# Kernel tuning notes

Measured on AMD Instinct MI355X. Metric: run time of the kernel, lower is better.

The kernel has to match this reference:

```python
import jax, jax.numpy as jnp
import numpy as np

N_NODES = 50000
N_EDGES = 800000
F_IN = 11
HID = 128
HEADS = 4
N_ACT = 6
NEG_SLOPE = 0.2


def _gat_layer(x, W, a_src, a_dst, b, src, dst, heads, out_dim):
    # x: [N, Fin]; W: [Fin, heads*out]; a_src/a_dst: [heads, out]; b: [heads*out]
    N = x.shape[0]
    h = (x @ W).reshape(N, heads, out_dim)                     # [N,H,C]
    alpha_src = jnp.einsum('nhc,hc->nh', h, a_src)             # [N,H]
    alpha_dst = jnp.einsum('nhc,hc->nh', h, a_dst)             # [N,H]
    e = jax.nn.leaky_relu(alpha_src[src] + alpha_dst[dst], NEG_SLOPE)  # [E,H]
    # segment softmax over incoming edges of each dst node
    m = jax.ops.segment_max(e, dst, num_segments=N)            # [N,H]
    ex = jnp.exp(e - m[dst])
    s = jax.ops.segment_sum(ex, dst, num_segments=N)           # [N,H]
    alpha = ex / s[dst]                                        # [E,H]
    msg = h[src] * alpha[..., None]                            # [E,H,C]
    agg = jax.ops.segment_sum(msg, dst, num_segments=N)        # [N,H,C]
    return agg.reshape(N, heads * out_dim) + b


def setup_inputs() -> dict:
    key = jax.random.key(0)
    ks = jax.random.split(key, 24)
    f32 = jnp.float32
    p = {}
    p['x'] = jax.random.normal(ks[0], (N_NODES, F_IN), dtype=f32)
    p['edge_index'] = jax.random.randint(ks[1], (2, N_EDGES), 0, N_NODES, dtype=jnp.int64)
    p['current_node_idx'] = 0
    def w(k, shape):
        return (jax.random.normal(k, shape, dtype=f32) * 0.1)
    p['W1'] = w(ks[2], (F_IN, HEADS * HID)); p['as1'] = w(ks[3], (HEADS, HID))
    p['ad1'] = w(ks[4], (HEADS, HID)); p['b1'] = jnp.zeros((HEADS * HID,), f32)
    p['W2'] = w(ks[5], (HEADS * HID, HEADS * HID)); p['as2'] = w(ks[6], (HEADS, HID))
    p['ad2'] = w(ks[7], (HEADS, HID)); p['b2'] = jnp.zeros((HEADS * HID,), f32)
    # layer 3: 512 -> 128, 1 head
    p['W3'] = w(ks[8], (HEADS * HID, HID)); p['as3'] = w(ks[9], (1, HID))
    p['ad3'] = w(ks[10], (1, HID)); p['b3'] = jnp.zeros((HID,), f32)
    # policy head
    p['pw1'] = w(ks[11], (HID, HID)); p['pb1'] = jnp.zeros((HID,), f32)
    p['pw2'] = w(ks[12], (HID, N_ACT)); p['pb2'] = jnp.zeros((N_ACT,), f32)
    # value head
    p['vw1'] = w(ks[13], (HID, HID)); p['vb1'] = jnp.zeros((HID,), f32)
    p['vw2'] = w(ks[14], (HID, 1)); p['vb2'] = jnp.zeros((1,), f32)
    return p


def reference(x, edge_index, current_node_idx,
              W1, as1, ad1, b1, W2, as2, ad2, b2, W3, as3, ad3, b3,
              pw1, pb1, pw2, pb2, vw1, vb1, vw2, vb2):
    src, dst = edge_index[0], edge_index[1]
    h = _gat_layer(x, W1, as1, ad1, b1, src, dst, HEADS, HID)
    h = jax.nn.elu(h)
    h = _gat_layer(h, W2, as2, ad2, b2, src, dst, HEADS, HID)
    h = jax.nn.elu(h)
    h = _gat_layer(h, W3, as3, ad3, b3, src, dst, 1, HID)      # [N, HID]
    graph_emb = h.mean(axis=0, keepdims=True)                  # [1, HID]
    combined = graph_emb + h[current_node_idx]                 # [1, HID]
    p = jax.nn.relu(combined @ pw1 + pb1) @ pw2 + pb2          # [1, N_ACT]
    v = jax.nn.relu(combined @ vw1 + vb1) @ vw2 + vb2          # [1, 1]
    return p, v
```

## Files before the change

kernel.cpp:

```cpp
#include <hip/hip_runtime.h>
#include <math.h>

#define NN 50000
#define NE 800000
#define F_IN 11
#define HID 128
#define NEG_SLOPE 0.2f

typedef __attribute__((ext_vector_type(8))) short short8;
typedef __attribute__((ext_vector_type(4))) float f32x4;

__device__ __forceinline__ float bf2f(ushort u) {
  return __uint_as_float(((unsigned)u) << 16);
}
__device__ __forceinline__ ushort f2bf(float f) {
  unsigned u = __float_as_uint(f);
  return (ushort)((u + 0x7fff + ((u >> 16) & 1)) >> 16);
}
__device__ __forceinline__ float lrelu(float x) { return x > 0.f ? x : NEG_SLOPE * x; }
__device__ __forceinline__ float elu1(float x) { return x > 0.f ? x : expm1f(x); }

#define MNEG (-1e30f)

__device__ __forceinline__ void wave_fence() {
  asm volatile("s_waitcnt lgkmcnt(0)" ::: "memory");
}

#define AS1 __attribute__((address_space(1)))
#define AS3 __attribute__((address_space(3)))

__global__ void k_deg(const int* __restrict__ ei, int* __restrict__ deg) {
  int e = blockIdx.x * blockDim.x + threadIdx.x;
  if (e < NE) atomicAdd(&deg[ei[NE + e]], 1);
}

__global__ void k_scan(const int* __restrict__ deg, int* __restrict__ row_ptr,
                       int* __restrict__ cursor) {
  const int T = 1024;
  const int CH = (NN + T - 1) / T;
  __shared__ int ssum[T];
  int t = threadIdx.x;
  int base = t * CH;
  int s = 0;
  for (int i = 0; i < CH; i++) {
    int idx = base + i;
    if (idx < NN) s += deg[idx];
  }
  ssum[t] = s;
  __syncthreads();
  for (int off = 1; off < T; off <<= 1) {
    int v = (t >= off) ? ssum[t - off] : 0;
    __syncthreads();
    ssum[t] += v;
    __syncthreads();
  }
  int run = ssum[t] - s;
  for (int i = 0; i < CH; i++) {
    int idx = base + i;
    if (idx < NN) {
      row_ptr[idx] = run;
      cursor[idx] = run;
      run += deg[idx];
    }
  }
  if (t == 0) row_ptr[NN] = ssum[T - 1];
}

__global__ void k_scatter(const int* __restrict__ ei, int* __restrict__ cursor,
                          int* __restrict__ csr_src) {
  int e = blockIdx.x * blockDim.x + threadIdx.x;
  if (e < NE) {
    int d = ei[NE + e];
    int pos = atomicAdd(&cursor[d], 1);
    csr_src[pos] = ei[e];
  }
}

__global__ void k_wt(const float* __restrict__ W, ushort* __restrict__ Wt, int K, int N) {
  __shared__ float tl[32][33];
  int bn = blockIdx.x * 32, bk = blockIdx.y * 32;
  int tx = threadIdx.x & 31, ty = threadIdx.x >> 5;
  for (int i = ty; i < 32; i += 8) tl[i][tx] = W[(size_t)(bk + i) * N + bn + tx];
  __syncthreads();
  for (int i = ty; i < 32; i += 8)
    Wt[(size_t)(bn + i) * K + bk + tx] = f2bf(tl[tx][i]);
}

__global__ void k_vsd(const float* __restrict__ W1, const float* __restrict__ as1,
                      const float* __restrict__ ad1, float* __restrict__ vs,
                      float* __restrict__ vd) {
  int t = threadIdx.x;
  if (t >= 88) return;
  int side = t & 1, kh = t >> 1;
  int k = kh >> 2, h = kh & 3;
  const float* av = side ? ad1 : as1;
  float s = 0.f;
  for (int c = 0; c < HID; c++) s += W1[k * 512 + h * HID + c] * av[h * HID + c];
  (side ? vd : vs)[kh] = s;
}

__global__ void k_ax(const float* __restrict__ x, const float* __restrict__ vs,
                     const float* __restrict__ vd, float* __restrict__ asrc,
                     float* __restrict__ adst) {
  int n = blockIdx.x * blockDim.x + threadIdx.x;
  if (n >= NN) return;
  float xr[F_IN];
#pragma unroll
  for (int k = 0; k < F_IN; k++) xr[k] = x[n * F_IN + k];
  float s[4] = {}, dd[4] = {};
#pragma unroll
  for (int k = 0; k < F_IN; k++)
#pragma unroll
    for (int h = 0; h < 4; h++) {
      s[h] += xr[k] * vs[k * 4 + h];
      dd[h] += xr[k] * vd[k * 4 + h];
    }
  *(f32x4*)(asrc + n * 4) = f32x4{s[0], s[1], s[2], s[3]};
  *(f32x4*)(adst + n * 4) = f32x4{dd[0], dd[1], dd[2], dd[3]};
}

__global__ __launch_bounds__(256) void k_aggpre(
    const float* __restrict__ x, const float* __restrict__ asrc,
    const float* __restrict__ adst, const int* __restrict__ row_ptr,
    const int* __restrict__ csr_src, float* __restrict__ P) {
  const int CAP = 64;
  __shared__ int src_c[4][CAP];
  __shared__ float ea[4][CAP * 4];
  int t = threadIdx.x, lane = t & 63, wv = t >> 6;
  int d = blockIdx.x * 4 + wv;
  int start = row_ptr[d], deg = row_ptr[d + 1] - start;
  int dcap = min(deg, CAP);
  for (int i = lane; i < dcap; i += 64) src_c[wv][i] = csr_src[start + i];
  wave_fence();
  int hh = lane & 3;
  float adh = adst[d * 4 + hh];
  float m = MNEG, s = 0.f;
  int deg4 = deg * 4;
  for (int i = lane; i < deg4; i += 64) {
    int k = i >> 2;
    int sn = (k < CAP) ? src_c[wv][k] : csr_src[start + k];
    float v = lrelu(asrc[sn * 4 + hh] + adh);
    if (k < CAP) ea[wv][i] = v;
    float nm = fmaxf(m, v);
    s = s * __expf(m - nm) + __expf(v - nm);
    m = nm;
  }
#pragma unroll
  for (int off = 4; off < 64; off <<= 1) {
    float m2 = __shfl_xor(m, off);
    float s2 = __shfl_xor(s, off);
    float nm = fmaxf(m, m2);
    s = s * __expf(m - nm) + s2 * __expf(m2 - nm);
    m = nm;
  }
  float sinv = (s > 0.f) ? 1.f / s : 0.f;
  int dc4 = dcap * 4;
  for (int i = lane; i < dc4; i += 64) ea[wv][i] = __expf(ea[wv][i] - m) * sinv;
  wave_fence();
  int hq = lane / F_IN;
  int k = lane - hq * F_IN;
  int h = hq & 3;
  float mh = __shfl(m, h), sih = __shfl(sinv, h);
  float adh2 = adst[d * 4 + h];
  float acc = 0.f;
  for (int e = 0; e < deg; e++) {
    int sn;
    float a;
    if (e < CAP) {
      sn = src_c[wv][e];
      a = ea[wv][e * 4 + h];
    } else {
      sn = csr_src[start + e];
      a = __expf(lrelu(asrc[sn * 4 + h] + adh2) - mh) * sih;
    }
    acc += a * x[sn * F_IN + k];
  }
  if (lane < 44) P[(size_t)d * 44 + lane] = acc;
}

__global__ __launch_bounds__(256) void k_gemm_l1(
    const float* __restrict__ P, const float* __restrict__ W1,
    const float* __restrict__ b1, ushort* __restrict__ out) {
  __shared__ float sW[F_IN * 512];
  __shared__ float sP[16][44];
  int t = threadIdx.x;
  for (int i = t; i < F_IN * 512; i += 256) sW[i] = W1[i];
  int n0 = blockIdx.x * 16;
  for (int i = t; i < 16 * 44; i += 256)
    sP[i / 44][i % 44] = P[(size_t)(n0 + i / 44) * 44 + (i % 44)];
  __syncthreads();
  int j0 = 2 * t;
  int h = j0 >> 7;
  float b0 = b1[j0], bb = b1[j0 + 1];
  float w0[F_IN], w1v[F_IN];
#pragma unroll
  for (int k = 0; k < F_IN; k++) {
    w0[k] = sW[k * 512 + j0];
    w1v[k] = sW[k * 512 + j0 + 1];
  }
  for (int nn = 0; nn < 16; nn++) {
    float a0 = b0, a1 = bb;
#pragma unroll
    for (int k = 0; k < F_IN; k++) {
      float pv = sP[nn][h * F_IN + k];
      a0 += pv * w0[k];
      a1 += pv * w1v[k];
    }
    a0 = elu1(a0);
    a1 = elu1(a1);
    unsigned pk = (unsigned)f2bf(a0) | ((unsigned)f2bf(a1) << 16);
    *(unsigned*)(out + (size_t)(n0 + nn) * 512 + j0) = pk;
  }
}

#define TM 128
#define TN 128
#define TK 64
__global__ __launch_bounds__(256) void k_mfma(const ushort* __restrict__ A,
                                              const ushort* __restrict__ Bt,
                                              ushort* __restrict__ C,
                                              int M, int N, int K) {
  __shared__ ushort lds[TM * TK + TN * TK];
  ushort* As = lds;
  ushort* Bs = lds + TM * TK;
  int tid = threadIdx.x;
  int lane = tid & 63, wv = tid >> 6;
  int wr = wv >> 1, wc = wv & 1;
  int bm0 = blockIdx.x * TM, bn0 = blockIdx.y * TN;
  int l15 = lane & 15, l4 = lane >> 4;
  f32x4 acc[4][4] = {};
  for (int k0 = 0; k0 < K; k0 += TK) {
#pragma unroll
    for (int it = 0; it < 4; ++it) {
      int chunk = it * 4 + wv;
      int pbase = chunk * 1024;
      int p = pbase + lane * 16;
      int prow = p >> 7;
      int lblk = ((p >> 4) & 7) ^ (prow & 7);
      int gr = bm0 + prow;
      gr = gr < M ? gr : M - 1;
      __builtin_amdgcn_global_load_lds(
          (const AS1 void*)(A + (size_t)gr * K + (k0 + lblk * 8)),
          (AS3 void*)((char*)As + pbase), 16, 0, 0);
      int gb = bn0 + prow;
      __builtin_amdgcn_global_load_lds(
          (const AS1 void*)(Bt + (size_t)gb * K + (k0 + lblk * 8)),
          (AS3 void*)((char*)Bs + pbase), 16, 0, 0);
    }
    __syncthreads();
#pragma unroll
    for (int kk = 0; kk < 2; ++kk) {
      int cb = kk * 4 + l4;
      short8 af[4], bfr[4];
#pragma unroll
      for (int m = 0; m < 4; ++m) {
        int row = wr * 64 + m * 16 + l15;
        af[m] = *(const short8*)((const char*)As + row * 128 + ((cb ^ (row & 7)) << 4));
      }
#pragma unroll
      for (int n = 0; n < 4; ++n) {
        int row = wc * 64 + n * 16 + l15;
        bfr[n] = *(const short8*)((const char*)Bs + row * 128 + ((cb ^ (row & 7)) << 4));
      }
#pragma unroll
      for (int m = 0; m < 4; ++m)
#pragma unroll
        for (int n = 0; n < 4; ++n)
          acc[m][n] = __builtin_amdgcn_mfma_f32_16x16x32_bf16(af[m], bfr[n], acc[m][n], 0, 0, 0);
    }
    __syncthreads();
  }
#pragma unroll
  for (int m = 0; m < 4; ++m) {
#pragma unroll
    for (int r = 0; r < 4; ++r) {
      int row = bm0 + wr * 64 + m * 16 + l4 * 4 + r;
      if (row < M) {
#pragma unroll
        for (int n = 0; n < 4; ++n) {
          int col = bn0 + wc * 64 + n * 16 + l15;
          C[(size_t)row * N + col] = f2bf(acc[m][n][r]);
        }
      }
    }
  }
}

template <int H>
__global__ void k_alpha(const ushort* __restrict__ h, const float* __restrict__ a_src,
                        const float* __restrict__ a_dst, float* __restrict__ asrc,
                        float* __restrict__ adst) {
  int t = threadIdx.x;
  int lane = t & 63;
  int n_g, h_g;
  if (H == 4) {
    n_g = blockIdx.x * 4 + (t >> 6);
    h_g = lane >> 4;
  } else {
    n_g = blockIdx.x * 16 + (t >> 4);
    h_g = 0;
  }
  if (n_g >= NN) return;
  int cl = lane & 15;
  short8 hv = *(const short8*)(h + (size_t)n_g * (H * 128) + h_g * 128 + cl * 8);
  const float* as = a_src + h_g * 128 + cl * 8;
  const float* ad = a_dst + h_g * 128 + cl * 8;
  float s1 = 0.f, s2 = 0.f;
#pragma unroll
  for (int j = 0; j < 8; j++) {
    float v = bf2f((ushort)hv[j]);
    s1 += v * as[j];
    s2 += v * ad[j];
  }
#pragma unroll
  for (int off = 1; off < 16; off <<= 1) {
    s1 += __shfl_xor(s1, off);
    s2 += __shfl_xor(s2, off);
  }
  if (cl == 0) {
    asrc[n_g * H + h_g] = s1;
    adst[n_g * H + h_g] = s2;
  }
}

__global__ __launch_bounds__(256) void k_agg4w(
    const ushort* __restrict__ h, const float* __restrict__ asrc,
    const float* __restrict__ adst, const int* __restrict__ row_ptr,
    const int* __restrict__ csr_src, const float* __restrict__ bias,
    ushort* __restrict__ out) {
  const int CAP = 64;
  __shared__ int src_c[4][CAP];
  __shared__ float ea[4][CAP * 4];
  int t = threadIdx.x, lane = t & 63, wv = t >> 6;
  int d = blockIdx.x * 4 + wv;
  int start = row_ptr[d], deg = row_ptr[d + 1] - start;
  int dcap = min(deg, CAP);
  for (int i = lane; i < dcap; i += 64) src_c[wv][i] = csr_src[start + i];
  wave_fence();
  int hh = lane & 3;
  float adh = adst[d * 4 + hh];
  float m = MNEG, s = 0.f;
  int deg4 = deg * 4;
  for (int i = lane; i < deg4; i += 64) {
    int k = i >> 2;
    int sn = (k < CAP) ? src_c[wv][k] : csr_src[start + k];
    float v = lrelu(asrc[sn * 4 + hh] + adh);
    if (k < CAP) ea[wv][i] = v;
    float nm = fmaxf(m, v);
    s = s * __expf(m - nm) + __expf(v - nm);
    m = nm;
  }
#pragma unroll
  for (int off = 4; off < 64; off <<= 1) {
    float m2 = __shfl_xor(m, off);
    float s2 = __shfl_xor(s, off);
    float nm = fmaxf(m, m2);
    s = s * __expf(m - nm) + s2 * __expf(m2 - nm);
    m = nm;
  }
  float sinv = (s > 0.f) ? 1.f / s : 0.f;
  int dc4 = dcap * 4;
  for (int i = lane; i < dc4; i += 64) ea[wv][i] = __expf(ea[wv][i] - m) * sinv;
  wave_fence();
  int hl = lane >> 4;
  float mh = __shfl(m, hl), sih = __shfl(sinv, hl);
  float adh2 = adst[d * 4 + hl];
  float acc[8] = {};
  for (int k = 0; k < deg; k++) {
    int sn;
    float a;
    if (k < CAP) {
      sn = src_c[wv][k];
      a = ea[wv][k * 4 + hl];
    } else {
      sn = csr_src[start + k];
      a = __expf(lrelu(asrc[sn * 4 + hl] + adh2) - mh) * sih;
    }
    short8 hv = *(const short8*)(h + (size_t)sn * 512 + lane * 8);
#pragma unroll
    for (int j = 0; j < 8; j++) acc[j] += a * bf2f((ushort)hv[j]);
  }
  const float* bp = bias + lane * 8;
  unsigned pk[4];
#pragma unroll
  for (int j = 0; j < 4; j++) {
    float o0 = elu1(acc[2 * j] + bp[2 * j]);
    float o1 = elu1(acc[2 * j + 1] + bp[2 * j + 1]);
    pk[j] = (unsigned)f2bf(o0) | ((unsigned)f2bf(o1) << 16);
  }
  *(uint4*)(out + (size_t)d * 512 + lane * 8) = make_uint4(pk[0], pk[1], pk[2], pk[3]);
}

__global__ __launch_bounds__(256) void k_agg1w(
    const ushort* __restrict__ h, const float* __restrict__ asrc,
    const float* __restrict__ adst, const int* __restrict__ row_ptr,
    const int* __restrict__ csr_src, const float* __restrict__ bias,
    ushort* __restrict__ out) {
  const int CAP = 64;
  __shared__ int src_c[4][CAP];
  __shared__ float ea[4][CAP];
  int t = threadIdx.x, lane = t & 63, wv = t >> 6;
  int d = blockIdx.x * 4 + wv;
  int start = row_ptr[d], deg = row_ptr[d + 1] - start;
  int dcap = min(deg, CAP);
  for (int i = lane; i < dcap; i += 64) src_c[wv][i] = csr_src[start + i];
  wave_fence();
  float adh = adst[d];
  float m = MNEG, s = 0.f;
  for (int i = lane; i < deg; i += 64) {
    int sn = (i < CAP) ? src_c[wv][i] : csr_src[start + i];
    float v = lrelu(asrc[sn] + adh);
    if (i < CAP) ea[wv][i] = v;
    float nm = fmaxf(m, v);
    s = s * __expf(m - nm) + __expf(v - nm);
    m = nm;
  }
#pragma unroll
  for (int off = 1; off < 64; off <<= 1) {
    float m2 = __shfl_xor(m, off);
    float s2 = __shfl_xor(s, off);
    float nm = fmaxf(m, m2);
    s = s * __expf(m - nm) + s2 * __expf(m2 - nm);
    m = nm;
  }
  float sinv = (s > 0.f) ? 1.f / s : 0.f;
  for (int i = lane; i < dcap; i += 64) ea[wv][i] = __expf(ea[wv][i] - m) * sinv;
  wave_fence();
  float acc0 = 0.f, acc1 = 0.f;
  for (int k = 0; k < deg; k++) {
    int sn;
    float a;
    if (k < CAP) {
      sn = src_c[wv][k];
      a = ea[wv][k];
    } else {
      sn = csr_src[start + k];
      a = __expf(lrelu(asrc[sn] + adh) - m) * sinv;
    }
    unsigned hv = *(const unsigned*)(h + (size_t)sn * 128 + lane * 2);
    acc0 += a * bf2f((ushort)(hv & 0xffff));
    acc1 += a * bf2f((ushort)(hv >> 16));
  }
  float o0 = acc0 + bias[lane * 2];
  float o1 = acc1 + bias[lane * 2 + 1];
  unsigned pk = (unsigned)f2bf(o0) | ((unsigned)f2bf(o1) << 16);
  *(unsigned*)(out + (size_t)d * 128 + lane * 2) = pk;
}

__global__ __launch_bounds__(256) void k_colsum(const ushort* __restrict__ h3,
                                                float* __restrict__ gsum) {
  __shared__ float partial[16 * 128];
  int t = threadIdx.x;
  int rg = t >> 4, cl = t & 15;
  int nb = gridDim.x;
  int per = (NN + nb - 1) / nb;
  int r0 = blockIdx.x * per, r1 = min(NN, r0 + per);
  float acc[8] = {};
  for (int r = r0 + rg; r < r1; r += 16) {
    short8 hv = *(const short8*)(h3 + (size_t)r * 128 + cl * 8);
#pragma unroll
    for (int j = 0; j < 8; j++) acc[j] += bf2f((ushort)hv[j]);
  }
#pragma unroll
  for (int j = 0; j < 8; j++) partial[rg * 128 + cl * 8 + j] = acc[j];
  __syncthreads();
  if (t < 128) {
    float s = 0.f;
    for (int q = 0; q < 16; q++) s += partial[q * 128 + t];
    atomicAdd(&gsum[t], s);
  }
}

__global__ void k_head(const float* __restrict__ gsum, const ushort* __restrict__ h3,
                       const int* __restrict__ curp, const float* __restrict__ pw1,
                       const float* __restrict__ pb1, const float* __restrict__ pw2,
                       const float* __restrict__ pb2, const float* __restrict__ vw1,
                       const float* __restrict__ vb1, const float* __restrict__ vw2,
                       const float* __restrict__ vb2, float* __restrict__ outp) {
  __shared__ float comb[HID], ph[HID], vh[HID];
  int t = threadIdx.x;
  int cur = curp[0];
  comb[t] = gsum[t] * (1.f / NN) + bf2f(h3[(size_t)cur * HID + t]);
  __syncthreads();
  float accp = pb1[t], accv = vb1[t];
  for (int k = 0; k < HID; k++) {
    float cv = comb[k];
    accp += cv * pw1[k * HID + t];
    accv += cv * vw1[k * HID + t];
  }
  ph[t] = fmaxf(accp, 0.f);
  vh[t] = fmaxf(accv, 0.f);
  __syncthreads();
  if (t < 6) {
    float a = pb2[t];
    for (int k = 0; k < HID; k++) a += ph[k] * pw2[k * 6 + t];
    outp[t] = a;
  }
  if (t == 6) {
    float a = vb2[0];
    for (int k = 0; k < HID; k++) a += vh[k] * vw2[k];
    outp[6] = a;
  }
}

extern "C" void kernel_launch(void* const* d_in, const int* in_sizes, int n_in,
                              void* d_out, int out_size, void* d_ws, size_t ws_size,
                              hipStream_t stream) {
  const float* x = (const float*)d_in[0];
  const int* ei = (const int*)d_in[1];
  const int* cur = (const int*)d_in[2];
  const float* W1 = (const float*)d_in[3];
  const float* as1 = (const float*)d_in[4];
  const float* ad1 = (const float*)d_in[5];
  const float* b1 = (const float*)d_in[6];
  const float* W2 = (const float*)d_in[7];
  const float* as2 = (const float*)d_in[8];
  const float* ad2 = (const float*)d_in[9];
  const float* b2 = (const float*)d_in[10];
  const float* W3 = (const float*)d_in[11];
  const float* as3 = (const float*)d_in[12];
  const float* ad3 = (const float*)d_in[13];
  const float* b3 = (const float*)d_in[14];
  const float* pw1 = (const float*)d_in[15];
  const float* pb1 = (const float*)d_in[16];
  const float* pw2 = (const float*)d_in[17];
  const float* pb2 = (const float*)d_in[18];
  const float* vw1 = (const float*)d_in[19];
  const float* vb1 = (const float*)d_in[20];
  const float* vw2 = (const float*)d_in[21];
  const float* vb2 = (const float*)d_in[22];
  float* out = (float*)d_out;

  char* w = (char*)d_ws;
  ushort* G = (ushort*)w;    w += (size_t)NN * 512 * 2;
  ushort* Abuf = (ushort*)w; w += (size_t)NN * 512 * 2;
  ushort* Wt2 = (ushort*)w;  w += (size_t)512 * 512 * 2;
  ushort* Wt3 = (ushort*)w;  w += (size_t)128 * 512 * 2;
  float* P = (float*)w;      w += (size_t)NN * 44 * 4;
  float* asrc = (float*)w;   w += (size_t)NN * 4 * 4;
  float* adst = (float*)w;   w += (size_t)NN * 4 * 4;
  int* deg = (int*)w;        w += (size_t)NN * 4;
  int* cursor = (int*)w;     w += (size_t)NN * 4;
  int* row_ptr = (int*)w;    w += (size_t)(NN + 1) * 4;
  int* csr_src = (int*)w;    w += (size_t)NE * 4;
  float* gsum = (float*)w;   w += (size_t)HID * 4;
  float* vs = (float*)w;     w += 44 * 4;
  float* vd = (float*)w;     w += 44 * 4;

  hipMemsetAsync(deg, 0, NN * 4, stream);
  hipMemsetAsync(gsum, 0, HID * 4, stream);

  k_deg<<<(NE + 255) / 256, 256, 0, stream>>>(ei, deg);
  k_scan<<<1, 1024, 0, stream>>>(deg, row_ptr, cursor);
  k_scatter<<<(NE + 255) / 256, 256, 0, stream>>>(ei, cursor, csr_src);

  k_wt<<<dim3(512 / 32, 512 / 32), 256, 0, stream>>>(W2, Wt2, 512, 512);
  k_wt<<<dim3(128 / 32, 512 / 32), 256, 0, stream>>>(W3, Wt3, 512, 128);

  const int GB = (NN + TM - 1) / TM;

  k_vsd<<<1, 128, 0, stream>>>(W1, as1, ad1, vs, vd);
  k_ax<<<(NN + 255) / 256, 256, 0, stream>>>(x, vs, vd, asrc, adst);
  k_aggpre<<<NN / 4, 256, 0, stream>>>(x, asrc, adst, row_ptr, csr_src, P);
  k_gemm_l1<<<NN / 16, 256, 0, stream>>>(P, W1, b1, Abuf);

  k_mfma<<<dim3(GB, 4), 256, 0, stream>>>(Abuf, Wt2, G, NN, 512, 512);
  k_alpha<4><<<(NN + 3) / 4, 256, 0, stream>>>(G, as2, ad2, asrc, adst);
  k_agg4w<<<NN / 4, 256, 0, stream>>>(G, asrc, adst, row_ptr, csr_src, b2, Abuf);

  k_mfma<<<dim3(GB, 1), 256, 0, stream>>>(Abuf, Wt3, G, NN, 128, 512);
  k_alpha<1><<<(NN + 15) / 16, 256, 0, stream>>>(G, as3, ad3, asrc, adst);
  k_agg1w<<<NN / 4, 256, 0, stream>>>(G, asrc, adst, row_ptr, csr_src, b3, Abuf);

  k_colsum<<<256, 256, 0, stream>>>(Abuf, gsum);
  k_head<<<1, 128, 0, stream>>>(gsum, Abuf, cur, pw1, pb1, pw2, pb2, vw1, vb1, vw2, vb2, out);
}
```

Before: 668.5 us.

## Fuse attention-logit computation into MFMA GEMM epilogue, remap blocks per XCD, unroll aggregation

The separate k_alpha kernels are removed. The attention source/destination dot products are now computed in the MFMA GEMM epilogue from the fp32 accumulators, reduced across lanes and waves through shared memory, and written directly. The GEMM grid becomes 1D with an XCD-aware block remap so that neighbouring tiles land on the same XCD for L2 reuse. The aggregation loops in k_agg4w and k_agg1w are unrolled by two with dual accumulators so more gathers are in flight. This saves a kernel launch and a full re-read of G per layer. In exchange it adds epilogue shuffles and extra registers, and the logits are now computed from unrounded fp32 values rather than from the bf16 output.

After: 680.0 us. Within noise of the previous version (+1.7%).

```diff
diff --git a/kernel.cpp b/kernel.cpp
--- a/kernel.cpp
+++ b/kernel.cpp
@@ -216,17 +216,25 @@
 #define TM 128
 #define TN 128
 #define TK 64
-__global__ __launch_bounds__(256) void k_mfma(const ushort* __restrict__ A,
-                                              const ushort* __restrict__ Bt,
-                                              ushort* __restrict__ C,
-                                              int M, int N, int K) {
+template <int H>
+__global__ __launch_bounds__(256) void k_mfma(
+    const ushort* __restrict__ A, const ushort* __restrict__ Bt,
+    ushort* __restrict__ C, const float* __restrict__ a_srcv,
+    const float* __restrict__ a_dstv, float* __restrict__ asrc,
+    float* __restrict__ adst, int M, int N, int K) {
   __shared__ ushort lds[TM * TK + TN * TK];
+  __shared__ float sal[128][2], sad[128][2];
   ushort* As = lds;
   ushort* Bs = lds + TM * TK;
   int tid = threadIdx.x;
   int lane = tid & 63, wv = tid >> 6;
   int wr = wv >> 1, wc = wv & 1;
-  int bm0 = blockIdx.x * TM, bn0 = blockIdx.y * TN;
+  int nwg = gridDim.x;
+  int q = nwg >> 3, rr = nwg & 7;
+  int xcd = blockIdx.x & 7, off8 = blockIdx.x >> 3;
+  int lid = (xcd < rr ? xcd * (q + 1) : rr * (q + 1) + (xcd - rr) * q) + off8;
+  int bm = lid / H, hy = lid - bm * H;
+  int bm0 = bm * TM, bn0 = hy * TN;
   int l15 = lane & 15, l4 = lane >> 4;
   f32x4 acc[4][4] = {};
   for (int k0 = 0; k0 < K; k0 += TK) {
@@ -284,42 +292,43 @@
       }
     }
   }
-}
-
-template <int H>
-__global__ void k_alpha(const ushort* __restrict__ h, const float* __restrict__ a_src,
-                        const float* __restrict__ a_dst, float* __restrict__ asrc,
-                        float* __restrict__ adst) {
-  int t = threadIdx.x;
-  int lane = t & 63;
-  int n_g, h_g;
-  if (H == 4) {
-    n_g = blockIdx.x * 4 + (t >> 6);
-    h_g = lane >> 4;
-  } else {
-    n_g = blockIdx.x * 16 + (t >> 4);
-    h_g = 0;
-  }
-  if (n_g >= NN) return;
-  int cl = lane & 15;
-  short8 hv = *(const short8*)(h + (size_t)n_g * (H * 128) + h_g * 128 + cl * 8);
-  const float* as = a_src + h_g * 128 + cl * 8;
-  const float* ad = a_dst + h_g * 128 + cl * 8;
-  float s1 = 0.f, s2 = 0.f;
-#pragma unroll
-  for (int j = 0; j < 8; j++) {
-    float v = bf2f((ushort)hv[j]);
-    s1 += v * as[j];
-    s2 += v * ad[j];
-  }
-#pragma unroll
-  for (int off = 1; off < 16; off <<= 1) {
-    s1 += __shfl_xor(s1, off);
-    s2 += __shfl_xor(s2, off);
-  }
-  if (cl == 0) {
-    asrc[n_g * H + h_g] = s1;
-    adst[n_g * H + h_g] = s2;
+  float asv[4], adv[4];
+#pragma unroll
+  for (int n = 0; n < 4; ++n) {
+    int c = hy * 128 + wc * 64 + n * 16 + l15;
+    asv[n] = a_srcv[c];
+    adv[n] = a_dstv[c];
+  }
+#pragma unroll
+  for (int m = 0; m < 4; ++m) {
+#pragma unroll
+    for (int r = 0; r < 4; ++r) {
+      float s1 = 0.f, s2 = 0.f;
+#pragma unroll
+      for (int n = 0; n < 4; ++n) {
+        float cv = acc[m][n][r];
+        s1 += cv * asv[n];
+        s2 += cv * adv[n];
+      }
+#pragma unroll
+      for (int off = 1; off < 16; off <<= 1) {
+        s1 += __shfl_xor(s1, off);
+        s2 += __shfl_xor(s2, off);
+      }
+      if (l15 == 0) {
+        int rb = wr * 64 + m * 16 + l4 * 4 + r;
+        sal[rb][wc] = s1;
+        sad[rb][wc] = s2;
+      }
+    }
+  }
+  __syncthreads();
+  if (tid < 128) {
+    int gr = bm0 + tid;
+    if (gr < M) {
+      asrc[gr * H + hy] = sal[tid][0] + sal[tid][1];
+      adst[gr * H + hy] = sad[tid][0] + sad[tid][1];
+    }
   }
 }
 
@@ -365,8 +374,33 @@
   int hl = lane >> 4;
   float mh = __shfl(m, hl), sih = __shfl(sinv, hl);
   float adh2 = adst[d * 4 + hl];
-  float acc[8] = {};
-  for (int k = 0; k < deg; k++) {
+  float acc0[8] = {}, acc1[8] = {};
+  int k = 0;
+  for (; k + 2 <= deg; k += 2) {
+    int sn0, sn1;
+    float a0, a1;
+    if (k < CAP) {
+      sn0 = src_c[wv][k];
+      a0 = ea[wv][k * 4 + hl];
+    } else {
+      sn0 = csr_src[start + k];
+      a0 = __expf(lrelu(asrc[sn0 * 4 + hl] + adh2) - mh) * sih;
+    }
+    if (k + 1 < CAP) {
+      sn1 = src_c[wv][k + 1];
+      a1 = ea[wv][(k + 1) * 4 + hl];
+    } else {
+      sn1 = csr_src[start + k + 1];
+      a1 = __expf(lrelu(asrc[sn1 * 4 + hl] + adh2) - mh) * sih;
+    }
+    short8 v0 = *(const short8*)(h + (size_t)sn0 * 512 + lane * 8);
+    short8 v1 = *(const short8*)(h + (size_t)sn1 * 512 + lane * 8);
+#pragma unroll
+    for (int j = 0; j < 8; j++) acc0[j] += a0 * bf2f((ushort)v0[j]);
+#pragma unroll
+    for (int j = 0; j < 8; j++) acc1[j] += a1 * bf2f((ushort)v1[j]);
+  }
+  if (k < deg) {
     int sn;
     float a;
     if (k < CAP) {
@@ -376,16 +410,16 @@
       sn = csr_src[start + k];
       a = __expf(lrelu(asrc[sn * 4 + hl] + adh2) - mh) * sih;
     }
-    short8 hv = *(const short8*)(h + (size_t)sn * 512 + lane * 8);
-#pragma unroll
-    for (int j = 0; j < 8; j++) acc[j] += a * bf2f((ushort)hv[j]);
+    short8 v0 = *(const short8*)(h + (size_t)sn * 512 + lane * 8);
+#pragma unroll
+    for (int j = 0; j < 8; j++) acc0[j] += a * bf2f((ushort)v0[j]);
   }
   const float* bp = bias + lane * 8;
   unsigned pk[4];
 #pragma unroll
   for (int j = 0; j < 4; j++) {
-    float o0 = elu1(acc[2 * j] + bp[2 * j]);
-    float o1 = elu1(acc[2 * j + 1] + bp[2 * j + 1]);
+    float o0 = elu1(acc0[2 * j] + acc1[2 * j] + bp[2 * j]);
+    float o1 = elu1(acc0[2 * j + 1] + acc1[2 * j + 1] + bp[2 * j + 1]);
     pk[j] = (unsigned)f2bf(o0) | ((unsigned)f2bf(o1) << 16);
   }
   *(uint4*)(out + (size_t)d * 512 + lane * 8) = make_uint4(pk[0], pk[1], pk[2], pk[3]);
@@ -426,23 +460,48 @@
   float sinv = (s > 0.f) ? 1.f / s : 0.f;
   for (int i = lane; i < dcap; i += 64) ea[wv][i] = __expf(ea[wv][i] - m) * sinv;
   wave_fence();
-  float acc0 = 0.f, acc1 = 0.f;
-  for (int k = 0; k < deg; k++) {
+  float a00 = 0.f, a01 = 0.f, a10 = 0.f, a11 = 0.f;
+  int k = 0;
+  for (; k + 2 <= deg; k += 2) {
+    int sn0, sn1;
+    float w0, w1;
+    if (k < CAP) {
+      sn0 = src_c[wv][k];
+      w0 = ea[wv][k];
+    } else {
+      sn0 = csr_src[start + k];
+      w0 = __expf(lrelu(asrc[sn0] + adh) - m) * sinv;
+    }
+    if (k + 1 < CAP) {
+      sn1 = src_c[wv][k + 1];
+      w1 = ea[wv][k + 1];
+    } else {
+      sn1 = csr_src[start + k + 1];
+      w1 = __expf(lrelu(asrc[sn1] + adh) - m) * sinv;
+    }
+    unsigned h0 = *(const unsigned*)(h + (size_t)sn0 * 128 + lane * 2);
+    unsigned h1 = *(const unsigned*)(h + (size_t)sn1 * 128 + lane * 2);
+    a00 += w0 * bf2f((ushort)(h0 & 0xffff));
+    a01 += w0 * bf2f((ushort)(h0 >> 16));
+    a10 += w1 * bf2f((ushort)(h1 & 0xffff));
+    a11 += w1 * bf2f((ushort)(h1 >> 16));
+  }
+  if (k < deg) {
     int sn;
-    float a;
+    float w0;
     if (k < CAP) {
       sn = src_c[wv][k];
-      a = ea[wv][k];
+      w0 = ea[wv][k];
     } else {
       sn = csr_src[start + k];
-      a = __expf(lrelu(asrc[sn] + adh) - m) * sinv;
-    }
-    unsigned hv = *(const unsigned*)(h + (size_t)sn * 128 + lane * 2);
-    acc0 += a * bf2f((ushort)(hv & 0xffff));
-    acc1 += a * bf2f((ushort)(hv >> 16));
-  }
-  float o0 = acc0 + bias[lane * 2];
-  float o1 = acc1 + bias[lane * 2 + 1];
+      w0 = __expf(lrelu(asrc[sn] + adh) - m) * sinv;
+    }
+    unsigned h0 = *(const unsigned*)(h + (size_t)sn * 128 + lane * 2);
+    a00 += w0 * bf2f((ushort)(h0 & 0xffff));
+    a01 += w0 * bf2f((ushort)(h0 >> 16));
+  }
+  float o0 = a00 + a10 + bias[lane * 2];
+  float o1 = a01 + a11 + bias[lane * 2 + 1];
   unsigned pk = (unsigned)f2bf(o0) | ((unsigned)f2bf(o1) << 16);
   *(unsigned*)(out + (size_t)d * 128 + lane * 2) = pk;
 }
@@ -564,12 +623,10 @@
   k_aggpre<<<NN / 4, 256, 0, stream>>>(x, asrc, adst, row_ptr, csr_src, P);
   k_gemm_l1<<<NN / 16, 256, 0, stream>>>(P, W1, b1, Abuf);
 
-  k_mfma<<<dim3(GB, 4), 256, 0, stream>>>(Abuf, Wt2, G, NN, 512, 512);
-  k_alpha<4><<<(NN + 3) / 4, 256, 0, stream>>>(G, as2, ad2, asrc, adst);
+  k_mfma<4><<<GB * 4, 256, 0, stream>>>(Abuf, Wt2, G, as2, ad2, asrc, adst, NN, 512, 512);
   k_agg4w<<<NN / 4, 256, 0, stream>>>(G, asrc, adst, row_ptr, csr_src, b2, Abuf);
 
-  k_mfma<<<dim3(GB, 1), 256, 0, stream>>>(Abuf, Wt3, G, NN, 128, 512);
-  k_alpha<1><<<(NN + 15) / 16, 256, 0, stream>>>(G, as3, ad3, asrc, adst);
+  k_mfma<1><<<GB, 256, 0, stream>>>(Abuf, Wt3, G, as3, ad3, asrc, adst, NN, 128, 512);
   k_agg1w<<<NN / 4, 256, 0, stream>>>(G, asrc, adst, row_ptr, csr_src, b3, Abuf);
 
   k_colsum<<<256, 256, 0, stream>>>(Abuf, gsum);
```

## Unroll edge gathers for memory-level parallelism and split layer-3 edges across lane groups

Applied to the files above, without the earlier changes.

The per-destination aggregation loops in the layer-1 pre-aggregation and the 4-head aggregation are unrolled by four, so four independent gathers are in flight per iteration, with separate accumulators in the 4-head kernel. The single-head aggregation is reorganised so each wave handles four edges at once: 16 lanes each read 16 bytes per edge, and the partial sums are combined with cross-lane shuffles. The layer-1 GEMM now processes 64 nodes per block instead of 16, spreading the shared-memory weight load over more rows. In exchange the kernels use more registers, which may lower occupancy, and the single-head kernel adds a shuffle reduction.

After: 671.6 us. No clear change (+0.5%).

```diff
diff --git a/kernel.cpp b/kernel.cpp
--- a/kernel.cpp
+++ b/kernel.cpp
@@ -163,18 +163,38 @@
   float mh = __shfl(m, h), sih = __shfl(sinv, h);
   float adh2 = adst[d * 4 + h];
   float acc = 0.f;
-  for (int e = 0; e < deg; e++) {
+#define GETP(i, SN, A)                                                \
+  do {                                                                \
+    int kk_ = e + (i);                                                \
+    if (kk_ < CAP) {                                                  \
+      SN = src_c[wv][kk_];                                            \
+      A = ea[wv][kk_ * 4 + h];                                        \
+    } else {                                                          \
+      SN = csr_src[start + kk_];                                      \
+      A = __expf(lrelu(asrc[SN * 4 + h] + adh2) - mh) * sih;          \
+    }                                                                 \
+  } while (0)
+  int e = 0;
+  for (; e + 4 <= deg; e += 4) {
+    int sn0, sn1, sn2, sn3;
+    float a0, a1, a2, a3;
+    GETP(0, sn0, a0);
+    GETP(1, sn1, a1);
+    GETP(2, sn2, a2);
+    GETP(3, sn3, a3);
+    float x0 = x[sn0 * F_IN + k];
+    float x1 = x[sn1 * F_IN + k];
+    float x2 = x[sn2 * F_IN + k];
+    float x3 = x[sn3 * F_IN + k];
+    acc += a0 * x0 + a1 * x1 + a2 * x2 + a3 * x3;
+  }
+  for (; e < deg; e++) {
     int sn;
     float a;
-    if (e < CAP) {
-      sn = src_c[wv][e];
-      a = ea[wv][e * 4 + h];
-    } else {
-      sn = csr_src[start + e];
-      a = __expf(lrelu(asrc[sn * 4 + h] + adh2) - mh) * sih;
-    }
+    GETP(0, sn, a);
     acc += a * x[sn * F_IN + k];
   }
+#undef GETP
   if (lane < 44) P[(size_t)d * 44 + lane] = acc;
 }
 
@@ -182,12 +202,14 @@
     const float* __restrict__ P, const float* __restrict__ W1,
     const float* __restrict__ b1, ushort* __restrict__ out) {
   __shared__ float sW[F_IN * 512];
-  __shared__ float sP[16][44];
+  __shared__ float sP[64][44];
   int t = threadIdx.x;
   for (int i = t; i < F_IN * 512; i += 256) sW[i] = W1[i];
-  int n0 = blockIdx.x * 16;
-  for (int i = t; i < 16 * 44; i += 256)
-    sP[i / 44][i % 44] = P[(size_t)(n0 + i / 44) * 44 + (i % 44)];
+  int n0 = blockIdx.x * 64;
+  for (int i = t; i < 64 * 44; i += 256) {
+    int nn = i / 44, kk = i % 44;
+    sP[nn][kk] = (n0 + nn < NN) ? P[(size_t)(n0 + nn) * 44 + kk] : 0.f;
+  }
   __syncthreads();
   int j0 = 2 * t;
   int h = j0 >> 7;
@@ -198,7 +220,8 @@
     w0[k] = sW[k * 512 + j0];
     w1v[k] = sW[k * 512 + j0 + 1];
   }
-  for (int nn = 0; nn < 16; nn++) {
+  for (int nn = 0; nn < 64; nn++) {
+    if (n0 + nn >= NN) break;
     float a0 = b0, a1 = bb;
 #pragma unroll
     for (int k = 0; k < F_IN; k++) {
@@ -365,27 +388,55 @@
   int hl = lane >> 4;
   float mh = __shfl(m, hl), sih = __shfl(sinv, hl);
   float adh2 = adst[d * 4 + hl];
-  float acc[8] = {};
-  for (int k = 0; k < deg; k++) {
+#define GET4(i, SN, A)                                                \
+  do {                                                                \
+    int kk_ = k + (i);                                                \
+    if (kk_ < CAP) {                                                  \
+      SN = src_c[wv][kk_];                                            \
+      A = ea[wv][kk_ * 4 + hl];                                       \
+    } else {                                                          \
+      SN = csr_src[start + kk_];                                      \
+      A = __expf(lrelu(asrc[SN * 4 + hl] + adh2) - mh) * sih;         \
+    }                                                                 \
+  } while (0)
+  float acc0[8] = {}, acc1[8] = {}, acc2[8] = {}, acc3[8] = {};
+  int k = 0;
+  for (; k + 4 <= deg; k += 4) {
+    int sn0, sn1, sn2, sn3;
+    float a0, a1, a2, a3;
+    GET4(0, sn0, a0);
+    GET4(1, sn1, a1);
+    GET4(2, sn2, a2);
+    GET4(3, sn3, a3);
+    short8 v0 = *(const short8*)(h + (size_t)sn0 * 512 + lane * 8);
+    short8 v1 = *(const short8*)(h + (size_t)sn1 * 512 + lane * 8);
+    short8 v2 = *(const short8*)(h + (size_t)sn2 * 512 + lane * 8);
+    short8 v3 = *(const short8*)(h + (size_t)sn3 * 512 + lane * 8);
+#pragma unroll
+    for (int j = 0; j < 8; j++) acc0[j] += a0 * bf2f((ushort)v0[j]);
+#pragma unroll
+    for (int j = 0; j < 8; j++) acc1[j] += a1 * bf2f((ushort)v1[j]);
+#pragma unroll
+    for (int j = 0; j < 8; j++) acc2[j] += a2 * bf2f((ushort)v2[j]);
+#pragma unroll
+    for (int j = 0; j < 8; j++) acc3[j] += a3 * bf2f((ushort)v3[j]);
+  }
+  for (; k < deg; k++) {
     int sn;
     float a;
-    if (k < CAP) {
-      sn = src_c[wv][k];
-      a = ea[wv][k * 4 + hl];
-    } else {
-      sn = csr_src[start + k];
-      a = __expf(lrelu(asrc[sn * 4 + hl] + adh2) - mh) * sih;
-    }
-    short8 hv = *(const short8*)(h + (size_t)sn * 512 + lane * 8);
-#pragma unroll
-    for (int j = 0; j < 8; j++) acc[j] += a * bf2f((ushort)hv[j]);
-  }
+    GET4(0, sn, a);
+    short8 v0 = *(const short8*)(h + (size_t)sn * 512 + lane * 8);
+#pragma unroll
+    for (int j = 0; j < 8; j++) acc0[j] += a * bf2f((ushort)v0[j]);
+  }
+#undef GET4
   const float* bp = bias + lane * 8;
   unsigned pk[4];
 #pragma unroll
   for (int j = 0; j < 4; j++) {
-    float o0 = elu1(acc[2 * j] + bp[2 * j]);
-    float o1 = elu1(acc[2 * j + 1] + bp[2 * j + 1]);
+    float o0 = elu1(acc0[2 * j] + acc1[2 * j] + acc2[2 * j] + acc3[2 * j] + bp[2 * j]);
+    float o1 = elu1(acc0[2 * j + 1] + acc1[2 * j + 1] + acc2[2 * j + 1] + acc3[2 * j + 1] +
+                    bp[2 * j + 1]);
     pk[j] = (unsigned)f2bf(o0) | ((unsigned)f2bf(o1) << 16);
   }
   *(uint4*)(out + (size_t)d * 512 + lane * 8) = make_uint4(pk[0], pk[1], pk[2], pk[3]);
@@ -400,6 +451,7 @@
   __shared__ int src_c[4][CAP];
   __shared__ float ea[4][CAP];
   int t = threadIdx.x, lane = t & 63, wv = t >> 6;
+  int slot = lane >> 4, cl = lane & 15;
   int d = blockIdx.x * 4 + wv;
   int start = row_ptr[d], deg = row_ptr[d + 1] - start;
   int dcap = min(deg, CAP);
@@ -426,25 +478,57 @@
   float sinv = (s > 0.f) ? 1.f / s : 0.f;
   for (int i = lane; i < dcap; i += 64) ea[wv][i] = __expf(ea[wv][i] - m) * sinv;
   wave_fence();
-  float acc0 = 0.f, acc1 = 0.f;
-  for (int k = 0; k < deg; k++) {
+#define GET1(KK, SN, A)                                               \
+  do {                                                                \
+    if ((KK) < CAP) {                                                 \
+      SN = src_c[wv][KK];                                             \
+      A = ea[wv][KK];                                                 \
+    } else {                                                          \
+      SN = csr_src[start + (KK)];                                     \
+      A = __expf(lrelu(asrc[SN] + adh) - m) * sinv;                   \
+    }                                                                 \
+  } while (0)
+  float acc0[8] = {}, acc1[8] = {};
+  int k = slot;
+  for (; k + 4 < deg; k += 8) {
+    int sn0, sn1;
+    float a0, a1;
+    GET1(k, sn0, a0);
+    GET1(k + 4, sn1, a1);
+    short8 v0 = *(const short8*)(h + (size_t)sn0 * 128 + cl * 8);
+    short8 v1 = *(const short8*)(h + (size_t)sn1 * 128 + cl * 8);
+#pragma unroll
+    for (int j = 0; j < 8; j++) acc0[j] += a0 * bf2f((ushort)v0[j]);
+#pragma unroll
+    for (int j = 0; j < 8; j++) acc1[j] += a1 * bf2f((ushort)v1[j]);
+  }
+  for (; k < deg; k += 4) {
     int sn;
     float a;
-    if (k < CAP) {
-      sn = src_c[wv][k];
-      a = ea[wv][k];
-    } else {
-      sn = csr_src[start + k];
-      a = __expf(lrelu(asrc[sn] + adh) - m) * sinv;
+    GET1(k, sn, a);
+    short8 v0 = *(const short8*)(h + (size_t)sn * 128 + cl * 8);
+#pragma unroll
+    for (int j = 0; j < 8; j++) acc0[j] += a * bf2f((ushort)v0[j]);
+  }
+#undef GET1
+#pragma unroll
+  for (int j = 0; j < 8; j++) {
+    float v = acc0[j] + acc1[j];
+    v += __shfl_xor(v, 16);
+    v += __shfl_xor(v, 32);
+    acc0[j] = v;
+  }
+  if (slot == 0) {
+    const float* bp = bias + cl * 8;
+    unsigned pk[4];
+#pragma unroll
+    for (int j = 0; j < 4; j++) {
+      float o0 = acc0[2 * j] + bp[2 * j];
+      float o1 = acc0[2 * j + 1] + bp[2 * j + 1];
+      pk[j] = (unsigned)f2bf(o0) | ((unsigned)f2bf(o1) << 16);
     }
-    unsigned hv = *(const unsigned*)(h + (size_t)sn * 128 + lane * 2);
-    acc0 += a * bf2f((ushort)(hv & 0xffff));
-    acc1 += a * bf2f((ushort)(hv >> 16));
-  }
-  float o0 = acc0 + bias[lane * 2];
-  float o1 = acc1 + bias[lane * 2 + 1];
-  unsigned pk = (unsigned)f2bf(o0) | ((unsigned)f2bf(o1) << 16);
-  *(unsigned*)(out + (size_t)d * 128 + lane * 2) = pk;
+    *(uint4*)(out + (size_t)d * 128 + cl * 8) = make_uint4(pk[0], pk[1], pk[2], pk[3]);
+  }
 }
 
 __global__ __launch_bounds__(256) void k_colsum(const ushort* __restrict__ h3,
@@ -562,7 +646,7 @@
   k_vsd<<<1, 128, 0, stream>>>(W1, as1, ad1, vs, vd);
   k_ax<<<(NN + 255) / 256, 256, 0, stream>>>(x, vs, vd, asrc, adst);
   k_aggpre<<<NN / 4, 256, 0, stream>>>(x, asrc, adst, row_ptr, csr_src, P);
-  k_gemm_l1<<<NN / 16, 256, 0, stream>>>(P, W1, b1, Abuf);
+  k_gemm_l1<<<(NN + 63) / 64, 256, 0, stream>>>(P, W1, b1, Abuf);
 
   k_mfma<<<dim3(GB, 4), 256, 0, stream>>>(Abuf, Wt2, G, NN, 512, 512);
   k_alpha<4><<<(NN + 3) / 4, 256, 0, stream>>>(G, as2, ad2, asrc, adst);
```
